# Performance work log

Hardware: AMD Instinct MI355X
Metric: run time of the kernel (lower is better)

## Reference

```python
import jax, jax.numpy as jnp
import numpy as np

N, T, NC, D = 256, 20, 1, 32
NF, Q, VSTEPS, HDYN = 16, 32, 10, 256
HDIM = NF * 64           # n_filt * 4**3
DT = 0.1
BETA = 1.0
LOG2PI = float(np.log(2.0 * np.pi))


def conv2d(x, w, b):
    # k=4, s=2, p=1 : halves spatial dims. x: [B,Cin,H,W], w: [Cout,Cin,4,4]
    y = jax.lax.conv_general_dilated(x, w, (2, 2), [(1, 1), (1, 1)],
                                     dimension_numbers=('NCHW', 'OIHW', 'NCHW'))
    return y + b[None, :, None, None]


def deconv2d(x, w, b):
    # stride-2 transposed conv, doubles spatial dims. w: [Cout,Cin,4,4]
    y = jax.lax.conv_transpose(x, w, (2, 2), 'SAME',
                               dimension_numbers=('NCHW', 'OIHW', 'NCHW'))
    return y + b[None, :, None, None]


def encode(x, C1, c1, C2, c2, C3, c3, Wm, bm, Wl, bl):
    h = jax.nn.relu(conv2d(x, C1, c1))
    h = jax.nn.relu(conv2d(h, C2, c2))
    h = jax.nn.relu(conv2d(h, C3, c3))   # [B, 4*NF, 4, 4]
    h = h.reshape(h.shape[0], -1)        # [B, HDIM]
    return h @ Wm + bm, h @ Wl + bl


def setup_inputs() -> dict:
    key = jax.random.key(0)
    ks = jax.random.split(key, 40)
    r = lambda i, shape, s=0.05: s * jax.random.normal(ks[i], shape, jnp.float32)
    inp = {
        'X': jax.random.uniform(ks[0], (N, T, NC, D, D), jnp.float32),
        'eps_s0': jax.random.normal(ks[1], (N, Q), jnp.float32),
        'eps_v0': jax.random.normal(ks[2], (N, Q), jnp.float32),
        # enc_s (input = 1 frame)
        'Cs1': r(3, (NF, NC, 4, 4)), 'cs1': jnp.zeros((NF,)),
        'Cs2': r(4, (2 * NF, NF, 4, 4)), 'cs2': jnp.zeros((2 * NF,)),
        'Cs3': r(5, (4 * NF, 2 * NF, 4, 4)), 'cs3': jnp.zeros((4 * NF,)),
        'Wsm': r(6, (HDIM, Q)), 'bsm': jnp.zeros((Q,)),
        'Wsl': r(7, (HDIM, Q), 0.01), 'bsl': -1.0 * jnp.ones((Q,)),
        # enc_v (input = v_steps frames stacked as channels)
        'Cv1': r(8, (NF, VSTEPS * NC, 4, 4)), 'cv1': jnp.zeros((NF,)),
        'Cv2': r(9, (2 * NF, NF, 4, 4)), 'cv2': jnp.zeros((2 * NF,)),
        'Cv3': r(10, (4 * NF, 2 * NF, 4, 4)), 'cv3': jnp.zeros((4 * NF,)),
        'Wvm': r(11, (HDIM, Q)), 'bvm': jnp.zeros((Q,)),
        'Wvl': r(12, (HDIM, Q), 0.01), 'bvl': -1.0 * jnp.ones((Q,)),
        # dynamics f : R^{2q} -> R^q (tanh MLP)
        'W1': r(13, (2 * Q, HDYN), 0.1), 'b1': jnp.zeros((HDYN,)),
        'W2': r(14, (HDYN, Q), 0.1), 'b2': jnp.zeros((Q,)),
        # fc3 + decoder
        'Wf': r(15, (Q, HDIM)), 'bf': jnp.zeros((HDIM,)),
        'D1': r(16, (2 * NF, 4 * NF, 4, 4)), 'd1': jnp.zeros((2 * NF,)),
        'D2': r(17, (NF, 2 * NF, 4, 4)), 'd2': jnp.zeros((NF,)),
        'D3': r(18, (NC, NF, 4, 4)), 'd3': jnp.zeros((NC,)),
        'Ndata': 10000,
    }
    return inp


def reference(X, eps_s0, eps_v0,
              Cs1, cs1, Cs2, cs2, Cs3, cs3, Wsm, bsm, Wsl, bsl,
              Cv1, cv1, Cv2, cv2, Cv3, cv3, Wvm, bvm, Wvl, bvl,
              W1, b1, W2, b2, Wf, bf, D1, d1, D2, d2, D3, d3, Ndata):
    Nb, Tt = X.shape[0], X.shape[1]
    # ---- encode z0 = [v0, s0]
    s0_mu, s0_lv = encode(X[:, 0], Cs1, cs1, Cs2, cs2, Cs3, cs3, Wsm, bsm, Wsl, bsl)
    xv = X[:, :VSTEPS].reshape(Nb, VSTEPS * NC, D, D)
    v0_mu, v0_lv = encode(xv, Cv1, cv1, Cv2, cv2, Cv3, cv3, Wvm, bvm, Wvl, bvl)
    s0 = s0_mu + eps_s0 * jnp.exp(s0_lv)
    v0 = v0_mu + eps_v0 * jnp.exp(v0_lv)
    # standard-normal density of the base noise (q dims each)
    logp0 = (-0.5 * jnp.sum(eps_s0 ** 2, -1) - 0.5 * Q * LOG2PI) + \
            (-0.5 * jnp.sum(eps_v0 ** 2, -1) - 0.5 * Q * LOG2PI)
    z0 = jnp.concatenate([v0, s0], axis=1)               # [N,2q]
    qz0_m = jnp.concatenate([v0_mu, s0_mu], axis=1)
    qz0_logv = jnp.concatenate([v0_lv, s0_lv], axis=1)

    # ---- augmented ODE rhs: dz = [f(z), v], dlogp = -tr(df/dv)
    # exact trace for the tanh MLP: J = W2^T diag(1-h^2) W1^T, so
    # tr_{i<q} J = (1-h^2) @ c with c_k = sum_{i<q} W1[i,k] * W2[k,i]
    c = jnp.sum(W1[:Q] * W2.T, axis=0)                   # [HDYN]

    def rhs(vs):
        h = jnp.tanh(vs @ W1 + b1)                       # [N,HDYN]
        dv = h @ W2 + b2                                 # [N,q]
        dvs = jnp.concatenate([dv, vs[:, :Q]], axis=1)   # [N,2q]
        tr = (1.0 - h * h) @ c                           # [N]
        return dvs, -tr

    def rk4_step(carry, _):
        z, lp = carry
        k1z, k1l = rhs(z)
        k2z, k2l = rhs(z + 0.5 * DT * k1z)
        k3z, k3l = rhs(z + 0.5 * DT * k2z)
        k4z, k4l = rhs(z + DT * k3z)
        z2 = z + (DT / 6.0) * (k1z + 2 * k2z + 2 * k3z + k4z)
        lp2 = lp + (DT / 6.0) * (k1l + 2 * k2l + 2 * k3l + k4l)
        return (z2, lp2), (z2, lp2)

    (_, _), (zs, lps) = jax.lax.scan(rk4_step, (z0, logp0), None, length=Tt - 1)
    zt = jnp.concatenate([z0[None], zs], axis=0)         # [T,N,2q]
    logp = jnp.concatenate([logp0[None], lps], axis=0)   # [T,N]
    ztL = jnp.transpose(zt, (1, 0, 2))[None]             # [1,N,T,2q] (L=1)
    logpL = logp.T[None]                                 # [1,N,T]

    # ---- decode positions s_t
    s = ztL[..., Q:].reshape(-1, Q) @ Wf + bf            # [N*T, HDIM]
    h = s.reshape(-1, 4 * NF, 4, 4)
    h = jax.nn.relu(deconv2d(h, D1, d1))                 # [N*T,2NF,8,8]
    h = jax.nn.relu(deconv2d(h, D2, d2))                 # [N*T,NF,16,16]
    Xrec = jax.nn.sigmoid(deconv2d(h, D3, d3))           # [N*T,NC,32,32]
    Xrec = Xrec.reshape(1, Nb, Tt, NC, D, D)

    # ---- ELBO
    log_pzt = -0.5 * jnp.sum(ztL ** 2, -1) - Q * LOG2PI  # N(0,I) over 2q dims
    kl_z = (logpL - log_pzt).sum(2).mean(0)              # [N]
    lhood_L = jnp.log(0.001 + Xrec) * X[None] + jnp.log(1.001 - Xrec) * (1.0 - X[None])
    lhood = lhood_L.sum((2, 3, 4, 5)).mean(0)            # [N]
    kl_w = 0.5 * (jnp.sum(W1 ** 2) + jnp.sum(W2 ** 2))
    Nd = jnp.float32(Ndata)
    lh = Nd * lhood.mean()
    klz = Nd * kl_z.mean()
    elbo = lh - klz - BETA * kl_w
    return Xrec, qz0_m, qz0_logv, ztL, elbo, lh, klz, BETA * kl_w


if __name__ == '__main__':
    outs = reference(**setup_inputs())
    print(outs[0].shape, float(outs[4]))
```

## Files before the change

### kernel.cpp

```cpp
#include <hip/hip_runtime.h>
#include <math.h>

#define N_S 256
#define T_S 20
#define D_S 32
#define NF_S 16
#define Q_S 32
#define HDYN_S 256
#define HDIM_S 1024
#define VSTEPS_S 10
#define DT_S 0.1f
#define LOG2PI_F 1.8378770664093453f

#define OUT_XREC 0
#define OUT_QM   5242880
#define OUT_QLV  5259264
#define OUT_ZT   5275648
#define OUT_SCAL 5603328

#define WS_A1    0
#define WS_A3    0
#define WS_WT2   32768
#define WS_WT3   40960
#define WS_A2    1048576
#define WS_M1    1048576
#define WS_C1    1114112
#define WS_S0MU  1572864
#define WS_S0LV  1581056
#define WS_V0MU  1589248
#define WS_V0LV  1597440
#define WS_LOGP  1605632
#define WS_LHOOD 1610752
#define WS_KLZ   1611008
#define WS_KLW   1611264
#define WS_TC    1611520
#define TC_S1 (WS_TC + 0)
#define TC_V1 (WS_TC + 256)
#define TC_S2 (WS_TC + 2816)
#define TC_V2 (WS_TC + 11008)
#define TC_S3 (WS_TC + 19200)
#define TC_V3 (WS_TC + 51968)

__device__ inline void enc_tr(const float* __restrict__ src, float* __restrict__ dst,
                              int e, int CI, int CO) {
    int co = e % CO; int r = e / CO; int tap = r & 15; int ci = r >> 4;
    dst[e] = src[(co * CI + ci) * 16 + tap];
}
__device__ inline void dec_tr(const float* __restrict__ src, float* __restrict__ dst,
                              int e, int CI, int CO) {
    int co = e % CO; int r = e / CO; int ci = r % CI; int tap = r / CI;
    dst[e] = src[(co * CI + ci) * 16 + tap];
}

__global__ __launch_bounds__(256) void prep_enc(
    const float* __restrict__ Cs1, const float* __restrict__ Cv1,
    const float* __restrict__ Cs2, const float* __restrict__ Cv2,
    const float* __restrict__ Cs3, const float* __restrict__ Cv3,
    float* __restrict__ ws)
{
    int idx = blockIdx.x * 256 + threadIdx.x;
    if (blockIdx.x == 0) ws[WS_LHOOD + threadIdx.x] = 0.f;
    if (idx < 256)        enc_tr(Cs1, ws + TC_S1, idx,          1, 16);
    else if (idx < 2816)  enc_tr(Cv1, ws + TC_V1, idx - 256,   10, 16);
    else if (idx < 11008) enc_tr(Cs2, ws + TC_S2, idx - 2816,  16, 32);
    else if (idx < 19200) enc_tr(Cv2, ws + TC_V2, idx - 11008, 16, 32);
    else if (idx < 51968) enc_tr(Cs3, ws + TC_S3, idx - 19200, 32, 64);
    else if (idx < 84736) enc_tr(Cv3, ws + TC_V3, idx - 51968, 32, 64);
}

template<int CIN>
__global__ __launch_bounds__(256) void conv1_lds(
    const float* __restrict__ x, const float* __restrict__ wt,
    const float* __restrict__ bias, float* __restrict__ out)
{
    __shared__ float xin[CIN * 630];
    __shared__ float wl[CIN * 256];
    __shared__ float bl[16];
    int b = blockIdx.x, yh = blockIdx.y, t = threadIdx.x;
    for (int e = t; e < CIN * 576; e += 256) {
        int ci = e / 576;
        int r = (e >> 5) - ci * 18;
        int cx = e & 31;
        int gy = yh * 16 - 1 + r;
        float v = (gy >= 0 && gy < 32) ? x[(size_t)b * 20480 + ci * 1024 + gy * 32 + cx] : 0.f;
        xin[ci * 630 + r * 35 + cx + 1] = v;
    }
    for (int e = t; e < CIN * 18; e += 256) {
        int ci = e / 18, r = e - ci * 18;
        xin[ci * 630 + r * 35 + 0] = 0.f;
        xin[ci * 630 + r * 35 + 33] = 0.f;
    }
    for (int e = t; e < CIN * 256; e += 256) wl[e] = wt[e];
    if (t < 16) bl[t] = bias[t];
    __syncthreads();

    int ocq = t >> 7, p = t & 127;
    int oyl = p >> 4, ox = p & 15;
    float acc[8];
    #pragma unroll
    for (int j = 0; j < 8; j++) acc[j] = bl[ocq * 8 + j];
    for (int ci = 0; ci < CIN; ci++) {
        const float* xc = xin + ci * 630;
        const float* wc = wl + ci * 256 + ocq * 8;
        #pragma unroll
        for (int ky = 0; ky < 4; ky++) {
            const float* xr = xc + (2 * oyl + ky) * 35;
            #pragma unroll
            for (int kx = 0; kx < 4; kx++) {
                float v = xr[2 * ox + kx];
                const float4* w4 = (const float4*)(wc + (ky * 4 + kx) * 16);
                float4 wa = w4[0], wb = w4[1];
                acc[0] = fmaf(v, wa.x, acc[0]);
                acc[1] = fmaf(v, wa.y, acc[1]);
                acc[2] = fmaf(v, wa.z, acc[2]);
                acc[3] = fmaf(v, wa.w, acc[3]);
                acc[4] = fmaf(v, wb.x, acc[4]);
                acc[5] = fmaf(v, wb.y, acc[5]);
                acc[6] = fmaf(v, wb.z, acc[6]);
                acc[7] = fmaf(v, wb.w, acc[7]);
            }
        }
    }
    int oy = yh * 8 + oyl;
    size_t ob = (size_t)b * 4096 + (size_t)(ocq * 8) * 256 + oy * 16 + ox;
    #pragma unroll
    for (int j = 0; j < 8; j++) out[ob + (size_t)j * 256] = fmaxf(acc[j], 0.f);
}

__global__ __launch_bounds__(256) void conv2_lds(
    const float* __restrict__ a1, const float* __restrict__ wt,
    const float* __restrict__ bias, float* __restrict__ out)
{
    __shared__ float xin[16 * 272];
    __shared__ float wl[4096];
    __shared__ float bl[16];
    int b = blockIdx.x, h = blockIdx.y, t = threadIdx.x;
    for (int e = t; e < 4096; e += 256) {
        int ci = e >> 8, r = e & 255, iy = r >> 4, ix = r & 15;
        xin[ci * 272 + iy * 17 + ix] = a1[(size_t)b * 4096 + e];
    }
    for (int e = t; e < 4096; e += 256) {
        int ci = e >> 8, r = e & 255, tap = r >> 4, oc = r & 15;
        wl[e] = wt[ci * 512 + tap * 32 + h * 16 + oc];
    }
    if (t < 16) bl[t] = bias[h * 16 + t];
    __syncthreads();

    int ocq = t >> 6, p = t & 63;
    int pa = p >> 3, pb = p & 7;
    float acc[4];
    #pragma unroll
    for (int j = 0; j < 4; j++) acc[j] = bl[ocq * 4 + j];
    for (int ci = 0; ci < 16; ci++) {
        const float* xc = xin + ci * 272;
        const float* wc = wl + ci * 256 + ocq * 4;
        #pragma unroll
        for (int ky = 0; ky < 4; ky++) {
            int iy = 2 * pa - 1 + ky;
            if ((unsigned)iy >= 16u) continue;
            const float* xr = xc + iy * 17;
            #pragma unroll
            for (int kx = 0; kx < 4; kx++) {
                int ix = 2 * pb - 1 + kx;
                if ((unsigned)ix >= 16u) continue;
                float v = xr[ix];
                float4 wv = *(const float4*)(wc + (ky * 4 + kx) * 16);
                acc[0] = fmaf(v, wv.x, acc[0]);
                acc[1] = fmaf(v, wv.y, acc[1]);
                acc[2] = fmaf(v, wv.z, acc[2]);
                acc[3] = fmaf(v, wv.w, acc[3]);
            }
        }
    }
    size_t ob = (size_t)b * 2048 + (size_t)(h * 16 + ocq * 4) * 64 + pa * 8 + pb;
    #pragma unroll
    for (int j = 0; j < 4; j++) out[ob + (size_t)j * 64] = fmaxf(acc[j], 0.f);
}

__global__ __launch_bounds__(256) void conv3_lds(
    const float* __restrict__ a2, const float* __restrict__ wt,
    const float* __restrict__ bias, float* __restrict__ out)
{
    __shared__ float xin[32 * 72];
    __shared__ float wl[16384];
    __shared__ float bl[32];
    int b = blockIdx.x, h = blockIdx.y, t = threadIdx.x;
    for (int e = t; e < 2048; e += 256) {
        int ci = e >> 6, r = e & 63, iy = r >> 3, ix = r & 7;
        xin[ci * 72 + iy * 9 + ix] = a2[(size_t)b * 2048 + e];
    }
    for (int e4 = t; e4 < 4096; e4 += 256) {
        int grp = e4 >> 3, c4 = e4 & 7;
        ((float4*)wl)[e4] = ((const float4*)(wt + grp * 64 + h * 32))[c4];
    }
    if (t < 32) bl[t] = bias[h * 32 + t];
    __syncthreads();

    int ocq = t >> 4, p = t & 15;
    int pa = p >> 2, pb = p & 3;
    float a0 = bl[ocq * 2], a1 = bl[ocq * 2 + 1];
    for (int ci = 0; ci < 32; ci++) {
        const float* xc = xin + ci * 72;
        const float* wc = wl + ci * 512 + ocq * 2;
        #pragma unroll
        for (int ky = 0; ky < 4; ky++) {
            int iy = 2 * pa - 1 + ky;
            if ((unsigned)iy >= 8u) continue;
            const float* xr = xc + iy * 9;
            #pragma unroll
            for (int kx = 0; kx < 4; kx++) {
                int ix = 2 * pb - 1 + kx;
                if ((unsigned)ix >= 8u) continue;
                float v = xr[ix];
                float2 wv = *(const float2*)(wc + (ky * 4 + kx) * 32);
                a0 = fmaf(v, wv.x, a0);
                a1 = fmaf(v, wv.y, a1);
            }
        }
    }
    size_t ob = (size_t)b * 1024 + (size_t)(h * 32 + ocq * 2) * 16 + pa * 4 + pb;
    out[ob] = fmaxf(a0, 0.f);
    out[ob + 16] = fmaxf(a1, 0.f);
}

__global__ __launch_bounds__(256) void fc_enc2(
    const float* __restrict__ h,
    const float* __restrict__ Wm, const float* __restrict__ bm,
    const float* __restrict__ Wl, const float* __restrict__ bl,
    float* __restrict__ mu, float* __restrict__ lv)
{
    __shared__ float pm[8][32], pl[8][32];
    int b = blockIdx.x, t = threadIdx.x;
    int q = t & 31, c = t >> 5;
    const float* hb = h + (size_t)b * HDIM_S + c * 128;
    const float* wmp = Wm + (c * 128) * Q_S + q;
    const float* wlp = Wl + (c * 128) * Q_S + q;
    float am = 0.f, al = 0.f;
    #pragma unroll 4
    for (int k = 0; k < 128; k++) {
        float hv = hb[k];
        am = fmaf(hv, wmp[k * Q_S], am);
        al = fmaf(hv, wlp[k * Q_S], al);
    }
    pm[c][q] = am; pl[c][q] = al;
    __syncthreads();
    if (t < 32) {
        float s = bm[t];
        #pragma unroll
        for (int c2 = 0; c2 < 8; c2++) s += pm[c2][t];
        mu[b * Q_S + t] = s;
    } else if (t < 64) {
        int qq = t - 32;
        float s = bl[qq];
        #pragma unroll
        for (int c2 = 0; c2 < 8; c2++) s += pl[c2][qq];
        lv[b * Q_S + qq] = s;
    }
}

__global__ __launch_bounds__(256) void m1_prep(
    const float* __restrict__ Wf, const float* __restrict__ bf,
    const float* __restrict__ D1, const float* __restrict__ d1,
    float* __restrict__ ws)
{
    int blk = blockIdx.x, t = threadIdx.x;
    if (blk < 64) {
        __shared__ float WfL[4096];
        __shared__ float D1L[4096];
        int j = blk >> 3, q4 = blk & 7;
        for (int e = t; e < 4096; e += 256) {
            int qq = e >> 10, k = e & 1023;
            WfL[e] = Wf[(size_t)(q4 * 4 + qq) * 1024 + k];
        }
        for (int e = t; e < 4096; e += 256) {
            int ocg = e >> 10, r = e & 1023;
            D1L[e] = D1[(size_t)(ocg * 8 + j) * 1024 + r];
        }
        __syncthreads();
        int p = t & 63, ocg = t >> 6;
        int y = p >> 3, x = p & 7;
        float acc[4] = {0.f, 0.f, 0.f, 0.f};
        #pragma unroll
        for (int sy = 0; sy < 2; sy++) {
            int ky = (y & 1) + 2 * sy;
            int iy = ((y + ky) >> 1) - 1;
            if ((unsigned)iy >= 4u) continue;
            #pragma unroll
            for (int sx = 0; sx < 2; sx++) {
                int kx = (x & 1) + 2 * sx;
                int ix = ((x + kx) >> 1) - 1;
                if ((unsigned)ix >= 4u) continue;
                const float* dl = D1L + ocg * 1024 + ky * 4 + kx;
                const float* wl = WfL + iy * 4 + ix;
                for (int ci = 0; ci < 64; ci++) {
                    float wv = dl[ci * 16];
                    int kb = ci * 16;
                    acc[0] = fmaf(wl[kb],        wv, acc[0]);
                    acc[1] = fmaf(wl[1024 + kb], wv, acc[1]);
                    acc[2] = fmaf(wl[2048 + kb], wv, acc[2]);
                    acc[3] = fmaf(wl[3072 + kb], wv, acc[3]);
                }
            }
        }
        float4 o4 = make_float4(acc[0], acc[1], acc[2], acc[3]);
        ((float4*)(ws + WS_M1))[blk * 256 + t] = o4;
    } else {
        __shared__ float bfL[1024];
        __shared__ float D1c[2048];
        int bb = blk - 64;
        for (int e = t; e < 1024; e += 256) bfL[e] = bf[e];
        for (int e = t; e < 2048; e += 256) D1c[e] = D1[(size_t)bb * 2048 + e];
        __syncthreads();
        int oidx = t >> 1, half = t & 1;
        int ocr = oidx >> 6, p = oidx & 63;
        int y = p >> 3, x = p & 7;
        float acc = 0.f;
        #pragma unroll
        for (int sy = 0; sy < 2; sy++) {
            int ky = (y & 1) + 2 * sy;
            int iy = ((y + ky) >> 1) - 1;
            if ((unsigned)iy >= 4u) continue;
            #pragma unroll
            for (int sx = 0; sx < 2; sx++) {
                int kx = (x & 1) + 2 * sx;
                int ix = ((x + kx) >> 1) - 1;
                if ((unsigned)ix >= 4u) continue;
                const float* dl = D1c + ocr * 1024 + half * 512 + ky * 4 + kx;
                const float* wl = bfL + half * 512 + iy * 4 + ix;
                for (int cc = 0; cc < 32; cc++)
                    acc = fmaf(wl[cc * 16], dl[cc * 16], acc);
            }
        }
        acc += __shfl_down(acc, 1, 64);
        if (half == 0) {
            int oc = bb * 2 + ocr;
            ws[WS_C1 + (oc & 7) * 256 + (oc >> 3) * 64 + p] = acc + d1[oc];
        }
    }
}

__global__ __launch_bounds__(256) void reparam_prep(
    const float* __restrict__ s0mu, const float* __restrict__ s0lv,
    const float* __restrict__ v0mu, const float* __restrict__ v0lv,
    const float* __restrict__ eps_s, const float* __restrict__ eps_v,
    const float* __restrict__ D2, const float* __restrict__ D3,
    float* __restrict__ ws,
    float* __restrict__ qm, float* __restrict__ qlv,
    float* __restrict__ ztL, float* __restrict__ logp)
{
    int n = blockIdx.x, t = threadIdx.x;
    int idx = n * 256 + t;
    if (idx < 8192)      dec_tr(D2, ws + WS_WT2, idx,        32, 16);
    else if (idx < 8448) dec_tr(D3, ws + WS_WT3, idx - 8192, 16, 1);
    if (t < 64) {
        int q = t & 31;
        float mu, lvv, ep;
        if (t < 32) { mu = v0mu[n*32+q]; lvv = v0lv[n*32+q]; ep = eps_v[n*32+q]; }
        else        { mu = s0mu[n*32+q]; lvv = s0lv[n*32+q]; ep = eps_s[n*32+q]; }
        float zv = fmaf(ep, expf(lvv), mu);
        qm[n*64 + t]  = mu;
        qlv[n*64 + t] = lvv;
        ztL[(size_t)n * T_S * 64 + t] = zv;
        float e2 = ep * ep;
        #pragma unroll
        for (int off = 32; off; off >>= 1) e2 += __shfl_down(e2, off, 64);
        if (t == 0) logp[n * T_S] = -0.5f * e2 - Q_S * LOG2PI_F;
    }
}

__global__ __launch_bounds__(256) void ode_kernel(
    const float* __restrict__ W1, const float* __restrict__ b1,
    const float* __restrict__ W2, const float* __restrict__ b2,
    float* __restrict__ ztL, float* __restrict__ logp)
{
    __shared__ float W2s[HDYN_S * Q_S];
    __shared__ float zeval[64];
    __shared__ float hsh[HDYN_S];
    __shared__ float dvred[HDYN_S];
    __shared__ float red4[4];
    int n = blockIdx.x;
    int t = threadIdx.x;

    for (int i = t; i < HDYN_S * Q_S; i += 256) W2s[i] = W2[i];
    float w1r[64];
    #pragma unroll
    for (int j = 0; j < 64; j++) w1r[j] = W1[j * HDYN_S + t];
    float b1r = b1[t];
    __syncthreads();
    float ck = 0.f;
    #pragma unroll
    for (int i = 0; i < Q_S; i++) ck = fmaf(w1r[i], W2s[t * Q_S + i], ck);

    size_t zoff = (size_t)n * T_S * 64;
    float zj = 0.f, ksumj = 0.f, zevalj = 0.f, lp = 0.f, lsum = 0.f;
    if (t < 64) { zj = ztL[zoff + t]; zevalj = zj; zeval[t] = zj; }
    if (t == 0) lp = logp[n * T_S];

    const float wc[4] = {1.f, 2.f, 2.f, 1.f};
    const float ac[3] = {0.5f * DT_S, 0.5f * DT_S, DT_S};

    for (int step = 1; step < T_S; step++) {
        for (int e = 0; e < 4; e++) {
            __syncthreads();
            float p0 = 0.f, p1 = 0.f, p2 = 0.f, p3 = 0.f;
            #pragma unroll
            for (int j = 0; j < 16; j++) {
                p0 = fmaf(zeval[j],      w1r[j],      p0);
                p1 = fmaf(zeval[j + 16], w1r[j + 16], p1);
                p2 = fmaf(zeval[j + 32], w1r[j + 32], p2);
                p3 = fmaf(zeval[j + 48], w1r[j + 48], p3);
            }
            float pre = b1r + ((p0 + p1) + (p2 + p3));
            float hk = tanhf(pre);
            hsh[t] = hk;
            float gk = (1.f - hk * hk) * ck;
            #pragma unroll
            for (int off = 32; off; off >>= 1) gk += __shfl_down(gk, off, 64);
            if ((t & 63) == 0) red4[t >> 6] = gk;
            __syncthreads();
            {
                int i = t & 31, p = t >> 5;
                float a0 = 0.f, a1 = 0.f;
                #pragma unroll
                for (int kk = 0; kk < 16; kk++) {
                    a0 = fmaf(hsh[p * 32 + kk],      W2s[(p * 32 + kk) * Q_S + i],      a0);
                    a1 = fmaf(hsh[p * 32 + 16 + kk], W2s[(p * 32 + 16 + kk) * Q_S + i], a1);
                }
                dvred[t] = a0 + a1;
            }
            __syncthreads();
            if (t < 64) {
                float tr = red4[0] + red4[1] + red4[2] + red4[3];
                float zv_shfl = __shfl(zevalj, (t >= 32) ? (t - 32) : t, 64);
                float kzv;
                if (t < 32) {
                    float dvi = b2[t];
                    #pragma unroll
                    for (int p = 0; p < 8; p++) dvi += dvred[p * 32 + t];
                    kzv = dvi;
                } else kzv = zv_shfl;
                if (e == 0) ksumj = kzv; else ksumj = fmaf(wc[e], kzv, ksumj);
                if (t == 0) { float kl = -tr; lsum = (e == 0) ? kl : fmaf(wc[e], kl, lsum); }
                if (e < 3) {
                    zevalj = fmaf(ac[e], kzv, zj);
                    zeval[t] = zevalj;
                } else {
                    zj = fmaf(DT_S / 6.f, ksumj, zj);
                    zevalj = zj; zeval[t] = zj;
                    ztL[zoff + step * 64 + t] = zj;
                    if (t == 0) { lp = fmaf(DT_S / 6.f, lsum, lp); logp[n * T_S + step] = lp; }
                }
            }
        }
    }
}

__global__ __launch_bounds__(256) void decoder5(
    const float* __restrict__ ztL, const float* __restrict__ M1L, const float* __restrict__ c1L,
    const float* __restrict__ wt2, const float* __restrict__ d2,
    const float* __restrict__ wt3, const float* __restrict__ d3,
    const float* __restrict__ X, float* __restrict__ Xrec, float* __restrict__ lhood)
{
    __shared__ float zs[32];
    __shared__ float regA[3600];
    __shared__ float regB[4160];
    __shared__ float sh4[4];
    float* h2f = regB;
    float* h1f = regA;
    float* xst = regA;
    const int bidx = blockIdx.x;
    const int t = threadIdx.x;
    const int wu = __builtin_amdgcn_readfirstlane(t >> 6);
    const int l = t & 63;
    const int py = wu >> 1, px = wu & 1;

    if (t < 32) zs[t] = ztL[(size_t)bidx * 64 + 32 + t];
    {
        float4 z4 = make_float4(0.f, 0.f, 0.f, 0.f);
        for (int e = t; e < 900; e += 256) ((float4*)regA)[e] = z4;
    }
    __syncthreads();

    {
        float acc[8];
        #pragma unroll
        for (int j = 0; j < 8; j++) acc[j] = c1L[j * 256 + t];
        const float4* M14 = (const float4*)M1L;
        #pragma unroll
        for (int q4 = 0; q4 < 8; q4++) {
            float4 z4 = *(const float4*)(zs + q4 * 4);
            #pragma unroll
            for (int j = 0; j < 8; j++) {
                float4 m = M14[(j * 8 + q4) * 256 + t];
                acc[j] = fmaf(z4.x, m.x, fmaf(z4.y, m.y, fmaf(z4.z, m.z, fmaf(z4.w, m.w, acc[j]))));
            }
        }
        int p = t & 63, ocg = t >> 6;
        int y = p >> 3, x = p & 7;
        float* hp = h1f + (y + 1) * 360 + (x + 1) * 36 + ocg * 8;
        float4 r0, r1;
        r0.x = fmaxf(acc[0], 0.f); r0.y = fmaxf(acc[1], 0.f);
        r0.z = fmaxf(acc[2], 0.f); r0.w = fmaxf(acc[3], 0.f);
        r1.x = fmaxf(acc[4], 0.f); r1.y = fmaxf(acc[5], 0.f);
        r1.z = fmaxf(acc[6], 0.f); r1.w = fmaxf(acc[7], 0.f);
        *(float4*)(hp)     = r0;
        *(float4*)(hp + 4) = r1;
    }
    __syncthreads();

    {
        int a = l >> 3, b = l & 7;
        float acc[16];
        #pragma unroll
        for (int j = 0; j < 16; j++) acc[j] = d2[j];
        #pragma unroll
        for (int sy = 0; sy < 2; sy++) {
            int ky = py + 2 * sy;
            int iyf = a + py + sy - 1;
            #pragma unroll
            for (int sx = 0; sx < 2; sx++) {
                int kx = px + 2 * sx;
                int ixf = b + px + sx - 1;
                const float4* ip4 = (const float4*)(h1f + (iyf + 1) * 360 + (ixf + 1) * 36);
                const float* wb = wt2 + (ky * 4 + kx) * 512;
                #pragma unroll 2
                for (int cc = 0; cc < 8; cc++) {
                    float4 v = ip4[cc];
                    float vv[4] = {v.x, v.y, v.z, v.w};
                    #pragma unroll
                    for (int r = 0; r < 4; r++) {
                        const float4* wq = (const float4*)(wb + (cc * 4 + r) * 16);
                        float4 w0 = wq[0], w1 = wq[1], w2 = wq[2], w3 = wq[3];
                        float vr = vv[r];
                        acc[0]  = fmaf(vr, w0.x, acc[0]);
                        acc[1]  = fmaf(vr, w0.y, acc[1]);
                        acc[2]  = fmaf(vr, w0.z, acc[2]);
                        acc[3]  = fmaf(vr, w0.w, acc[3]);
                        acc[4]  = fmaf(vr, w1.x, acc[4]);
                        acc[5]  = fmaf(vr, w1.y, acc[5]);
                        acc[6]  = fmaf(vr, w1.z, acc[6]);
                        acc[7]  = fmaf(vr, w1.w, acc[7]);
                        acc[8]  = fmaf(vr, w2.x, acc[8]);
                        acc[9]  = fmaf(vr, w2.y, acc[9]);
                        acc[10] = fmaf(vr, w2.z, acc[10]);
                        acc[11] = fmaf(vr, w2.w, acc[11]);
                        acc[12] = fmaf(vr, w3.x, acc[12]);
                        acc[13] = fmaf(vr, w3.y, acc[13]);
                        acc[14] = fmaf(vr, w3.z, acc[14]);
                        acc[15] = fmaf(vr, w3.w, acc[15]);
                    }
                }
            }
        }
        float* hq = h2f + (2 * a + py) * 260 + (2 * b + px) * 16;
        #pragma unroll
        for (int j = 0; j < 4; j++) {
            float4 r;
            r.x = fmaxf(acc[j*4+0], 0.f);
            r.y = fmaxf(acc[j*4+1], 0.f);
            r.z = fmaxf(acc[j*4+2], 0.f);
            r.w = fmaxf(acc[j*4+3], 0.f);
            *(float4*)(hq + j * 4) = r;
        }
    }
    __syncthreads();

    {
        int oy2 = l >> 2, b3 = l & 3;
        float acc[4];
        float d30 = d3[0];
        #pragma unroll
        for (int k = 0; k < 4; k++) acc[k] = d30;
        #pragma unroll
        for (int sy = 0; sy < 2; sy++) {
            int ky = py + 2 * sy;
            int iy = oy2 + py + sy - 1;
            if ((unsigned)iy >= 16u) continue;
            #pragma unroll
            for (int sx = 0; sx < 2; sx++) {
                int kx = px + 2 * sx;
                int cx = px + sx - 1;
                const float* wvp = wt3 + (ky * 4 + kx) * 16;
                #pragma unroll
                for (int k = 0; k < 4; k++) {
                    int ix = b3 + 4 * k + cx;
                    if ((unsigned)ix >= 16u) continue;
                    const float4* in4 = (const float4*)(h2f + iy * 260 + ix * 16);
                    #pragma unroll
                    for (int cc = 0; cc < 4; cc++) {
                        float4 v = in4[cc];
                        float4 wq = ((const float4*)wvp)[cc];
                        acc[k] = fmaf(v.x, wq.x, acc[k]);
                        acc[k] = fmaf(v.y, wq.y, acc[k]);
                        acc[k] = fmaf(v.z, wq.z, acc[k]);
                        acc[k] = fmaf(v.w, wq.w, acc[k]);
                    }
                }
            }
        }
        int oy = 2 * oy2 + py;
        #pragma unroll
        for (int k = 0; k < 4; k++) {
            int ox = 2 * (b3 + 4 * k) + px;
            xst[oy * 36 + ox] = 1.f / (1.f + expf(-acc[k]));
        }
    }
    __syncthreads();

    {
        int row = t >> 3, col = (t & 7) * 4;
        float4 xr4 = *(const float4*)(xst + row * 36 + col);
        *(float4*)(Xrec + (size_t)bidx * 1024 + t * 4) = xr4;
        float4 xi4 = *(const float4*)(X + (size_t)bidx * 1024 + t * 4);
        float ll = 0.f;
        ll += logf(0.001f + xr4.x) * xi4.x + logf(1.001f - xr4.x) * (1.f - xi4.x);
        ll += logf(0.001f + xr4.y) * xi4.y + logf(1.001f - xr4.y) * (1.f - xi4.y);
        ll += logf(0.001f + xr4.z) * xi4.z + logf(1.001f - xr4.z) * (1.f - xi4.z);
        ll += logf(0.001f + xr4.w) * xi4.w + logf(1.001f - xr4.w) * (1.f - xi4.w);
        #pragma unroll
        for (int off = 32; off; off >>= 1) ll += __shfl_down(ll, off, 64);
        if ((t & 63) == 0) sh4[t >> 6] = ll;
    }
    __syncthreads();
    if (t == 0) atomicAdd(&lhood[bidx / T_S], sh4[0] + sh4[1] + sh4[2] + sh4[3]);
}

__global__ __launch_bounds__(64) void klz_kernel(
    const float* __restrict__ ztL, const float* __restrict__ logp, float* __restrict__ klz)
{
    int n = blockIdx.x, t = threadIdx.x;
    float v = 0.f;
    if (t < T_S) {
        const float* z = ztL + ((size_t)n * T_S + t) * 64;
        float s2 = 0.f;
        #pragma unroll
        for (int j = 0; j < 64; j++) s2 = fmaf(z[j], z[j], s2);
        v = logp[n * T_S + t] - (-0.5f * s2 - Q_S * LOG2PI_F);
    }
    #pragma unroll
    for (int off = 32; off; off >>= 1) v += __shfl_down(v, off, 64);
    if (t == 0) klz[n] = v;
}

__global__ __launch_bounds__(256) void final2(
    const float* __restrict__ lhood, const float* __restrict__ klz,
    const float* __restrict__ W1, const float* __restrict__ W2,
    const int* __restrict__ Ndata, float* __restrict__ outs)
{
    __shared__ float shA[4], shB[4], shC[4];
    int t = threadIdx.x;
    float a = lhood[t];
    float b = klz[t];
    float c = 0.f;
    for (int i = t; i < 64 * HDYN_S; i += 256) c = fmaf(W1[i], W1[i], c);
    for (int i = t; i < HDYN_S * Q_S; i += 256) c = fmaf(W2[i], W2[i], c);
    #pragma unroll
    for (int off = 32; off; off >>= 1) {
        a += __shfl_down(a, off, 64);
        b += __shfl_down(b, off, 64);
        c += __shfl_down(c, off, 64);
    }
    if ((t & 63) == 0) { shA[t >> 6] = a; shB[t >> 6] = b; shC[t >> 6] = c; }
    __syncthreads();
    if (t == 0) {
        float Nd = (float)Ndata[0];
        float lh = Nd * ((shA[0] + shA[1] + shA[2] + shA[3]) / 256.f);
        float kz = Nd * ((shB[0] + shB[1] + shB[2] + shB[3]) / 256.f);
        float bkw = 0.5f * (shC[0] + shC[1] + shC[2] + shC[3]);
        outs[0] = lh - kz - bkw;
        outs[1] = lh;
        outs[2] = kz;
        outs[3] = bkw;
    }
}

extern "C" void kernel_launch(void* const* d_in, const int* in_sizes, int n_in,
                              void* d_out, int out_size, void* d_ws, size_t ws_size,
                              hipStream_t stream) {
    const float* X      = (const float*)d_in[0];
    const float* eps_s0 = (const float*)d_in[1];
    const float* eps_v0 = (const float*)d_in[2];
    const float* Cs1 = (const float*)d_in[3],  *cs1 = (const float*)d_in[4];
    const float* Cs2 = (const float*)d_in[5],  *cs2 = (const float*)d_in[6];
    const float* Cs3 = (const float*)d_in[7],  *cs3 = (const float*)d_in[8];
    const float* Wsm = (const float*)d_in[9],  *bsm = (const float*)d_in[10];
    const float* Wsl = (const float*)d_in[11], *bsl = (const float*)d_in[12];
    const float* Cv1 = (const float*)d_in[13], *cv1 = (const float*)d_in[14];
    const float* Cv2 = (const float*)d_in[15], *cv2 = (const float*)d_in[16];
    const float* Cv3 = (const float*)d_in[17], *cv3 = (const float*)d_in[18];
    const float* Wvm = (const float*)d_in[19], *bvm = (const float*)d_in[20];
    const float* Wvl = (const float*)d_in[21], *bvl = (const float*)d_in[22];
    const float* W1  = (const float*)d_in[23], *b1  = (const float*)d_in[24];
    const float* W2  = (const float*)d_in[25], *b2  = (const float*)d_in[26];
    const float* Wf  = (const float*)d_in[27], *bf  = (const float*)d_in[28];
    const float* D1  = (const float*)d_in[29], *d1  = (const float*)d_in[30];
    const float* D2  = (const float*)d_in[31], *d2  = (const float*)d_in[32];
    const float* D3  = (const float*)d_in[33], *d3  = (const float*)d_in[34];
    const int*   Ndata = (const int*)d_in[35];

    float* out = (float*)d_out;
    float* ws  = (float*)d_ws;

    prep_enc<<<331, 256, 0, stream>>>(Cs1, Cv1, Cs2, Cv2, Cs3, Cv3, ws);

    conv1_lds<1><<<dim3(256, 2), 256, 0, stream>>>(X, ws + TC_S1, cs1, ws + WS_A1);
    conv2_lds<<<dim3(256, 2), 256, 0, stream>>>(ws + WS_A1, ws + TC_S2, cs2, ws + WS_A2);
    conv3_lds<<<dim3(256, 2), 256, 0, stream>>>(ws + WS_A2, ws + TC_S3, cs3, ws + WS_A3);
    fc_enc2<<<256, 256, 0, stream>>>(ws + WS_A3, Wsm, bsm, Wsl, bsl, ws + WS_S0MU, ws + WS_S0LV);

    conv1_lds<10><<<dim3(256, 2), 256, 0, stream>>>(X, ws + TC_V1, cv1, ws + WS_A1);
    conv2_lds<<<dim3(256, 2), 256, 0, stream>>>(ws + WS_A1, ws + TC_V2, cv2, ws + WS_A2);
    conv3_lds<<<dim3(256, 2), 256, 0, stream>>>(ws + WS_A2, ws + TC_V3, cv3, ws + WS_A3);
    fc_enc2<<<256, 256, 0, stream>>>(ws + WS_A3, Wvm, bvm, Wvl, bvl, ws + WS_V0MU, ws + WS_V0LV);

    m1_prep<<<80, 256, 0, stream>>>(Wf, bf, D1, d1, ws);

    reparam_prep<<<256, 256, 0, stream>>>(ws + WS_S0MU, ws + WS_S0LV, ws + WS_V0MU, ws + WS_V0LV,
                                          eps_s0, eps_v0, D2, D3, ws,
                                          out + OUT_QM, out + OUT_QLV,
                                          out + OUT_ZT, ws + WS_LOGP);

    ode_kernel<<<256, 256, 0, stream>>>(W1, b1, W2, b2, out + OUT_ZT, ws + WS_LOGP);

    decoder5<<<5120, 256, 0, stream>>>(out + OUT_ZT, ws + WS_M1, ws + WS_C1,
                                       ws + WS_WT2, d2, ws + WS_WT3, d3,
                                       X, out + OUT_XREC, ws + WS_LHOOD);

    klz_kernel<<<256, 64, 0, stream>>>(out + OUT_ZT, ws + WS_LOGP, ws + WS_KLZ);
    final2<<<1, 256, 0, stream>>>(ws + WS_LHOOD, ws + WS_KLZ, W1, W2, Ndata,
                                  out + OUT_SCAL);
}
```

Before: 502.4 us.

## Merge s/v encoder branches into shared launches and fold KL into ODE kernel

The two encoder branches (single-frame s and stacked-frame v) now run in combined conv1/conv2/conv3/fc kernels, with a grid dimension selecting the branch. The s-branch activations go to scratch space in the output buffer so both branches can run at the same time. The m1_prep work is folded into reparam_prep, and the KL-z reduction is computed inside the ODE integration loop, which removes the klz kernel. conv1 and conv2 also stop staging weights in LDS and read them straight from global memory with wave-uniform offsets, trading LDS traffic for scalar or cached loads.

```diff
diff --git a/kernel.cpp b/kernel.cpp
--- a/kernel.cpp
+++ b/kernel.cpp
@@ -18,11 +18,15 @@
 #define OUT_ZT   5275648
 #define OUT_SCAL 5603328
 
-#define WS_A1    0
-#define WS_A3    0
+#define OS_A1S   0
+#define OS_A2S   1048576
+#define OS_A3S   1572864
+
+#define WS_A1V   0
+#define WS_A3V   0
 #define WS_WT2   32768
 #define WS_WT3   40960
-#define WS_A2    1048576
+#define WS_A2V   1048576
 #define WS_M1    1048576
 #define WS_C1    1114112
 #define WS_S0MU  1572864
@@ -68,16 +72,20 @@
     else if (idx < 84736) enc_tr(Cv3, ws + TC_V3, idx - 51968, 32, 64);
 }
 
-template<int CIN>
-__global__ __launch_bounds__(256) void conv1_lds(
-    const float* __restrict__ x, const float* __restrict__ wt,
-    const float* __restrict__ bias, float* __restrict__ out)
-{
-    __shared__ float xin[CIN * 630];
-    __shared__ float wl[CIN * 256];
-    __shared__ float bl[16];
+__global__ __launch_bounds__(256) void conv1_both(
+    const float* __restrict__ x,
+    const float* __restrict__ wts, const float* __restrict__ bs, float* __restrict__ outs,
+    const float* __restrict__ wtv, const float* __restrict__ bv, float* __restrict__ outv)
+{
+    __shared__ float xin[10 * 630];
+    int sel = blockIdx.z;
+    int cin = sel ? 10 : 1;
+    const float* wt = sel ? wtv : wts;
+    const float* bias = sel ? bv : bs;
+    float* out = sel ? outv : outs;
+
     int b = blockIdx.x, yh = blockIdx.y, t = threadIdx.x;
-    for (int e = t; e < CIN * 576; e += 256) {
+    for (int e = t; e < cin * 576; e += 256) {
         int ci = e / 576;
         int r = (e >> 5) - ci * 18;
         int cx = e & 31;
@@ -85,23 +93,23 @@
         float v = (gy >= 0 && gy < 32) ? x[(size_t)b * 20480 + ci * 1024 + gy * 32 + cx] : 0.f;
         xin[ci * 630 + r * 35 + cx + 1] = v;
     }
-    for (int e = t; e < CIN * 18; e += 256) {
+    for (int e = t; e < cin * 18; e += 256) {
         int ci = e / 18, r = e - ci * 18;
         xin[ci * 630 + r * 35 + 0] = 0.f;
         xin[ci * 630 + r * 35 + 33] = 0.f;
     }
-    for (int e = t; e < CIN * 256; e += 256) wl[e] = wt[e];
-    if (t < 16) bl[t] = bias[t];
-    __syncthreads();
-
-    int ocq = t >> 7, p = t & 127;
+    __syncthreads();
+
+    int ocq = __builtin_amdgcn_readfirstlane(t >> 7);
+    int p = t & 127;
     int oyl = p >> 4, ox = p & 15;
+    const float* wg = wt + ocq * 8;
     float acc[8];
     #pragma unroll
-    for (int j = 0; j < 8; j++) acc[j] = bl[ocq * 8 + j];
-    for (int ci = 0; ci < CIN; ci++) {
+    for (int j = 0; j < 8; j++) acc[j] = bias[ocq * 8 + j];
+    for (int ci = 0; ci < cin; ci++) {
         const float* xc = xin + ci * 630;
-        const float* wc = wl + ci * 256 + ocq * 8;
+        const float* wc = wg + ci * 256;
         #pragma unroll
         for (int ky = 0; ky < 4; ky++) {
             const float* xr = xc + (2 * oyl + ky) * 35;
@@ -109,15 +117,15 @@
             for (int kx = 0; kx < 4; kx++) {
                 float v = xr[2 * ox + kx];
                 const float4* w4 = (const float4*)(wc + (ky * 4 + kx) * 16);
-                float4 wa = w4[0], wb = w4[1];
+                float4 wa = w4[0], wb2 = w4[1];
                 acc[0] = fmaf(v, wa.x, acc[0]);
                 acc[1] = fmaf(v, wa.y, acc[1]);
                 acc[2] = fmaf(v, wa.z, acc[2]);
                 acc[3] = fmaf(v, wa.w, acc[3]);
-                acc[4] = fmaf(v, wb.x, acc[4]);
-                acc[5] = fmaf(v, wb.y, acc[5]);
-                acc[6] = fmaf(v, wb.z, acc[6]);
-                acc[7] = fmaf(v, wb.w, acc[7]);
+                acc[4] = fmaf(v, wb2.x, acc[4]);
+                acc[5] = fmaf(v, wb2.y, acc[5]);
+                acc[6] = fmaf(v, wb2.z, acc[6]);
+                acc[7] = fmaf(v, wb2.w, acc[7]);
             }
         }
     }
@@ -127,33 +135,36 @@
     for (int j = 0; j < 8; j++) out[ob + (size_t)j * 256] = fmaxf(acc[j], 0.f);
 }
 
-__global__ __launch_bounds__(256) void conv2_lds(
-    const float* __restrict__ a1, const float* __restrict__ wt,
-    const float* __restrict__ bias, float* __restrict__ out)
+__global__ __launch_bounds__(256) void conv2_both(
+    const float* __restrict__ a1s, const float* __restrict__ wts, const float* __restrict__ bsb,
+    float* __restrict__ outs,
+    const float* __restrict__ a1v, const float* __restrict__ wtv, const float* __restrict__ bvb,
+    float* __restrict__ outv)
 {
     __shared__ float xin[16 * 272];
-    __shared__ float wl[4096];
-    __shared__ float bl[16];
+    int sel = blockIdx.z;
+    const float* a1 = sel ? a1v : a1s;
+    const float* wt = sel ? wtv : wts;
+    const float* bias = sel ? bvb : bsb;
+    float* out = sel ? outv : outs;
+
     int b = blockIdx.x, h = blockIdx.y, t = threadIdx.x;
     for (int e = t; e < 4096; e += 256) {
         int ci = e >> 8, r = e & 255, iy = r >> 4, ix = r & 15;
         xin[ci * 272 + iy * 17 + ix] = a1[(size_t)b * 4096 + e];
     }
-    for (int e = t; e < 4096; e += 256) {
-        int ci = e >> 8, r = e & 255, tap = r >> 4, oc = r & 15;
-        wl[e] = wt[ci * 512 + tap * 32 + h * 16 + oc];
-    }
-    if (t < 16) bl[t] = bias[h * 16 + t];
-    __syncthreads();
-
-    int ocq = t >> 6, p = t & 63;
+    __syncthreads();
+
+    int ocq = __builtin_amdgcn_readfirstlane(t >> 6);
+    int p = t & 63;
     int pa = p >> 3, pb = p & 7;
+    int hbase = h * 16 + ocq * 4;
     float acc[4];
     #pragma unroll
-    for (int j = 0; j < 4; j++) acc[j] = bl[ocq * 4 + j];
+    for (int j = 0; j < 4; j++) acc[j] = bias[hbase + j];
     for (int ci = 0; ci < 16; ci++) {
         const float* xc = xin + ci * 272;
-        const float* wc = wl + ci * 256 + ocq * 4;
+        const float* wc = wt + ci * 512 + hbase;
         #pragma unroll
         for (int ky = 0; ky < 4; ky++) {
             int iy = 2 * pa - 1 + ky;
@@ -164,7 +175,7 @@
                 int ix = 2 * pb - 1 + kx;
                 if ((unsigned)ix >= 16u) continue;
                 float v = xr[ix];
-                float4 wv = *(const float4*)(wc + (ky * 4 + kx) * 16);
+                float4 wv = *(const float4*)(wc + (ky * 4 + kx) * 32);
                 acc[0] = fmaf(v, wv.x, acc[0]);
                 acc[1] = fmaf(v, wv.y, acc[1]);
                 acc[2] = fmaf(v, wv.z, acc[2]);
@@ -172,18 +183,26 @@
             }
         }
     }
-    size_t ob = (size_t)b * 2048 + (size_t)(h * 16 + ocq * 4) * 64 + pa * 8 + pb;
+    size_t ob = (size_t)b * 2048 + (size_t)(hbase) * 64 + pa * 8 + pb;
     #pragma unroll
     for (int j = 0; j < 4; j++) out[ob + (size_t)j * 64] = fmaxf(acc[j], 0.f);
 }
 
-__global__ __launch_bounds__(256) void conv3_lds(
-    const float* __restrict__ a2, const float* __restrict__ wt,
-    const float* __restrict__ bias, float* __restrict__ out)
+__global__ __launch_bounds__(256) void conv3_both(
+    const float* __restrict__ a2s, const float* __restrict__ wts, const float* __restrict__ bsb,
+    float* __restrict__ outs,
+    const float* __restrict__ a2v, const float* __restrict__ wtv, const float* __restrict__ bvb,
+    float* __restrict__ outv)
 {
     __shared__ float xin[32 * 72];
     __shared__ float wl[16384];
     __shared__ float bl[32];
+    int sel = blockIdx.z;
+    const float* a2 = sel ? a2v : a2s;
+    const float* wt = sel ? wtv : wts;
+    const float* bias = sel ? bvb : bsb;
+    float* out = sel ? outv : outs;
+
     int b = blockIdx.x, h = blockIdx.y, t = threadIdx.x;
     for (int e = t; e < 2048; e += 256) {
         int ci = e >> 6, r = e & 63, iy = r >> 3, ix = r & 7;
@@ -223,14 +242,26 @@
     out[ob + 16] = fmaxf(a1, 0.f);
 }
 
-__global__ __launch_bounds__(256) void fc_enc2(
-    const float* __restrict__ h,
-    const float* __restrict__ Wm, const float* __restrict__ bm,
-    const float* __restrict__ Wl, const float* __restrict__ bl,
-    float* __restrict__ mu, float* __restrict__ lv)
+__global__ __launch_bounds__(256) void fc_both(
+    const float* __restrict__ hs, const float* __restrict__ hv,
+    const float* __restrict__ Wsm, const float* __restrict__ bsm,
+    const float* __restrict__ Wsl, const float* __restrict__ bsl,
+    const float* __restrict__ Wvm, const float* __restrict__ bvm,
+    const float* __restrict__ Wvl, const float* __restrict__ bvl,
+    float* __restrict__ mus, float* __restrict__ lvs,
+    float* __restrict__ muv, float* __restrict__ lvv)
 {
     __shared__ float pm[8][32], pl[8][32];
-    int b = blockIdx.x, t = threadIdx.x;
+    int sel = blockIdx.x >> 8;
+    int b = blockIdx.x & 255, t = threadIdx.x;
+    const float* h  = sel ? hv : hs;
+    const float* Wm = sel ? Wvm : Wsm;
+    const float* bm = sel ? bvm : bsm;
+    const float* Wl = sel ? Wvl : Wsl;
+    const float* bl = sel ? bvl : bsl;
+    float* mu = sel ? muv : mus;
+    float* lv = sel ? lvv : lvs;
+
     int q = t & 31, c = t >> 5;
     const float* hb = h + (size_t)b * HDIM_S + c * 128;
     const float* wmp = Wm + (c * 128) * Q_S + q;
@@ -238,9 +269,9 @@
     float am = 0.f, al = 0.f;
     #pragma unroll 4
     for (int k = 0; k < 128; k++) {
-        float hv = hb[k];
-        am = fmaf(hv, wmp[k * Q_S], am);
-        al = fmaf(hv, wlp[k * Q_S], al);
+        float hv2 = hb[k];
+        am = fmaf(hv2, wmp[k * Q_S], am);
+        al = fmaf(hv2, wlp[k * Q_S], al);
     }
     pm[c][q] = am; pl[c][q] = al;
     __syncthreads();
@@ -258,23 +289,30 @@
     }
 }
 
-__global__ __launch_bounds__(256) void m1_prep(
+__global__ __launch_bounds__(256) void reparam_prep(
+    const float* __restrict__ s0mu, const float* __restrict__ s0lv,
+    const float* __restrict__ v0mu, const float* __restrict__ v0lv,
+    const float* __restrict__ eps_s, const float* __restrict__ eps_v,
     const float* __restrict__ Wf, const float* __restrict__ bf,
     const float* __restrict__ D1, const float* __restrict__ d1,
-    float* __restrict__ ws)
-{
-    int blk = blockIdx.x, t = threadIdx.x;
-    if (blk < 64) {
-        __shared__ float WfL[4096];
-        __shared__ float D1L[4096];
-        int j = blk >> 3, q4 = blk & 7;
+    const float* __restrict__ D2, const float* __restrict__ D3,
+    float* __restrict__ ws,
+    float* __restrict__ qm, float* __restrict__ qlv,
+    float* __restrict__ ztL, float* __restrict__ logp)
+{
+    __shared__ float shA[4096];
+    __shared__ float shB[4096];
+    int n = blockIdx.x, t = threadIdx.x;
+
+    if (n < 64) {
+        int j = n >> 3, q4 = n & 7;
         for (int e = t; e < 4096; e += 256) {
             int qq = e >> 10, k = e & 1023;
-            WfL[e] = Wf[(size_t)(q4 * 4 + qq) * 1024 + k];
+            shA[e] = Wf[(size_t)(q4 * 4 + qq) * 1024 + k];
         }
         for (int e = t; e < 4096; e += 256) {
             int ocg = e >> 10, r = e & 1023;
-            D1L[e] = D1[(size_t)(ocg * 8 + j) * 1024 + r];
+            shB[e] = D1[(size_t)(ocg * 8 + j) * 1024 + r];
         }
         __syncthreads();
         int p = t & 63, ocg = t >> 6;
@@ -290,8 +328,8 @@
                 int kx = (x & 1) + 2 * sx;
                 int ix = ((x + kx) >> 1) - 1;
                 if ((unsigned)ix >= 4u) continue;
-                const float* dl = D1L + ocg * 1024 + ky * 4 + kx;
-                const float* wl = WfL + iy * 4 + ix;
+                const float* dl = shB + ocg * 1024 + ky * 4 + kx;
+                const float* wl = shA + iy * 4 + ix;
                 for (int ci = 0; ci < 64; ci++) {
                     float wv = dl[ci * 16];
                     int kb = ci * 16;
@@ -302,14 +340,11 @@
                 }
             }
         }
-        float4 o4 = make_float4(acc[0], acc[1], acc[2], acc[3]);
-        ((float4*)(ws + WS_M1))[blk * 256 + t] = o4;
-    } else {
-        __shared__ float bfL[1024];
-        __shared__ float D1c[2048];
-        int bb = blk - 64;
-        for (int e = t; e < 1024; e += 256) bfL[e] = bf[e];
-        for (int e = t; e < 2048; e += 256) D1c[e] = D1[(size_t)bb * 2048 + e];
+        ((float4*)(ws + WS_M1))[n * 256 + t] = make_float4(acc[0], acc[1], acc[2], acc[3]);
+    } else if (n < 80) {
+        int bb = n - 64;
+        for (int e = t; e < 1024; e += 256) shA[e] = bf[e];
+        for (int e = t; e < 2048; e += 256) shB[e] = D1[(size_t)bb * 2048 + e];
         __syncthreads();
         int oidx = t >> 1, half = t & 1;
         int ocr = oidx >> 6, p = oidx & 63;
@@ -325,8 +360,8 @@
                 int kx = (x & 1) + 2 * sx;
                 int ix = ((x + kx) >> 1) - 1;
                 if ((unsigned)ix >= 4u) continue;
-                const float* dl = D1c + ocr * 1024 + half * 512 + ky * 4 + kx;
-                const float* wl = bfL + half * 512 + iy * 4 + ix;
+                const float* dl = shB + ocr * 1024 + half * 512 + ky * 4 + kx;
+                const float* wl = shA + half * 512 + iy * 4 + ix;
                 for (int cc = 0; cc < 32; cc++)
                     acc = fmaf(wl[cc * 16], dl[cc * 16], acc);
             }
@@ -336,30 +371,20 @@
             int oc = bb * 2 + ocr;
             ws[WS_C1 + (oc & 7) * 256 + (oc >> 3) * 64 + p] = acc + d1[oc];
         }
-    }
-}
-
-__global__ __launch_bounds__(256) void reparam_prep(
-    const float* __restrict__ s0mu, const float* __restrict__ s0lv,
-    const float* __restrict__ v0mu, const float* __restrict__ v0lv,
-    const float* __restrict__ eps_s, const float* __restrict__ eps_v,
-    const float* __restrict__ D2, const float* __restrict__ D3,
-    float* __restrict__ ws,
-    float* __restrict__ qm, float* __restrict__ qlv,
-    float* __restrict__ ztL, float* __restrict__ logp)
-{
-    int n = blockIdx.x, t = threadIdx.x;
-    int idx = n * 256 + t;
-    if (idx < 8192)      dec_tr(D2, ws + WS_WT2, idx,        32, 16);
-    else if (idx < 8448) dec_tr(D3, ws + WS_WT3, idx - 8192, 16, 1);
+    } else if (n < 113) {
+        int idx = (n - 80) * 256 + t;
+        if (idx < 8192)      dec_tr(D2, ws + WS_WT2, idx,        32, 16);
+        else if (idx < 8448) dec_tr(D3, ws + WS_WT3, idx - 8192, 16, 1);
+    }
+
     if (t < 64) {
         int q = t & 31;
-        float mu, lvv, ep;
-        if (t < 32) { mu = v0mu[n*32+q]; lvv = v0lv[n*32+q]; ep = eps_v[n*32+q]; }
-        else        { mu = s0mu[n*32+q]; lvv = s0lv[n*32+q]; ep = eps_s[n*32+q]; }
-        float zv = fmaf(ep, expf(lvv), mu);
+        float mu, lvv2, ep;
+        if (t < 32) { mu = v0mu[n*32+q]; lvv2 = v0lv[n*32+q]; ep = eps_v[n*32+q]; }
+        else        { mu = s0mu[n*32+q]; lvv2 = s0lv[n*32+q]; ep = eps_s[n*32+q]; }
+        float zv = fmaf(ep, expf(lvv2), mu);
         qm[n*64 + t]  = mu;
-        qlv[n*64 + t] = lvv;
+        qlv[n*64 + t] = lvv2;
         ztL[(size_t)n * T_S * 64 + t] = zv;
         float e2 = ep * ep;
         #pragma unroll
@@ -371,7 +396,8 @@
 __global__ __launch_bounds__(256) void ode_kernel(
     const float* __restrict__ W1, const float* __restrict__ b1,
     const float* __restrict__ W2, const float* __restrict__ b2,
-    float* __restrict__ ztL, float* __restrict__ logp)
+    float* __restrict__ ztL, const float* __restrict__ logp,
+    float* __restrict__ klz)
 {
     __shared__ float W2s[HDYN_S * Q_S];
     __shared__ float zeval[64];
@@ -392,9 +418,16 @@
     for (int i = 0; i < Q_S; i++) ck = fmaf(w1r[i], W2s[t * Q_S + i], ck);
 
     size_t zoff = (size_t)n * T_S * 64;
-    float zj = 0.f, ksumj = 0.f, zevalj = 0.f, lp = 0.f, lsum = 0.f;
+    float zj = 0.f, ksumj = 0.f, zevalj = 0.f, lp = 0.f, lsum = 0.f, klacc = 0.f;
     if (t < 64) { zj = ztL[zoff + t]; zevalj = zj; zeval[t] = zj; }
     if (t == 0) lp = logp[n * T_S];
+
+    if (t < 64) {
+        float e2 = zj * zj;
+        #pragma unroll
+        for (int off = 32; off; off >>= 1) e2 += __shfl_down(e2, off, 64);
+        if (t == 0) klacc += lp - (-0.5f * e2 - Q_S * LOG2PI_F);
+    }
 
     const float wc[4] = {1.f, 2.f, 2.f, 1.f};
     const float ac[3] = {0.5f * DT_S, 0.5f * DT_S, DT_S};
@@ -448,11 +481,16 @@
                     zj = fmaf(DT_S / 6.f, ksumj, zj);
                     zevalj = zj; zeval[t] = zj;
                     ztL[zoff + step * 64 + t] = zj;
-                    if (t == 0) { lp = fmaf(DT_S / 6.f, lsum, lp); logp[n * T_S + step] = lp; }
+                    if (t == 0) lp = fmaf(DT_S / 6.f, lsum, lp);
+                    float e2 = zj * zj;
+                    #pragma unroll
+                    for (int off = 32; off; off >>= 1) e2 += __shfl_down(e2, off, 64);
+                    if (t == 0) klacc += lp - (-0.5f * e2 - Q_S * LOG2PI_F);
                 }
             }
         }
     }
+    if (t == 0) klz[n] = klacc;
 }
 
 __global__ __launch_bounds__(256) void decoder5(
@@ -625,23 +663,6 @@
     if (t == 0) atomicAdd(&lhood[bidx / T_S], sh4[0] + sh4[1] + sh4[2] + sh4[3]);
 }
 
-__global__ __launch_bounds__(64) void klz_kernel(
-    const float* __restrict__ ztL, const float* __restrict__ logp, float* __restrict__ klz)
-{
-    int n = blockIdx.x, t = threadIdx.x;
-    float v = 0.f;
-    if (t < T_S) {
-        const float* z = ztL + ((size_t)n * T_S + t) * 64;
-        float s2 = 0.f;
-        #pragma unroll
-        for (int j = 0; j < 64; j++) s2 = fmaf(z[j], z[j], s2);
-        v = logp[n * T_S + t] - (-0.5f * s2 - Q_S * LOG2PI_F);
-    }
-    #pragma unroll
-    for (int off = 32; off; off >>= 1) v += __shfl_down(v, off, 64);
-    if (t == 0) klz[n] = v;
-}
-
 __global__ __launch_bounds__(256) void final2(
     const float* __restrict__ lhood, const float* __restrict__ klz,
     const float* __restrict__ W1, const float* __restrict__ W2,
@@ -701,32 +722,37 @@
     float* out = (float*)d_out;
     float* ws  = (float*)d_ws;
 
+    float* a1s = out + OS_A1S;
+    float* a2s = out + OS_A2S;
+    float* a3s = out + OS_A3S;
+
     prep_enc<<<331, 256, 0, stream>>>(Cs1, Cv1, Cs2, Cv2, Cs3, Cv3, ws);
 
-    conv1_lds<1><<<dim3(256, 2), 256, 0, stream>>>(X, ws + TC_S1, cs1, ws + WS_A1);
-    conv2_lds<<<dim3(256, 2), 256, 0, stream>>>(ws + WS_A1, ws + TC_S2, cs2, ws + WS_A2);
-    conv3_lds<<<dim3(256, 2), 256, 0, stream>>>(ws + WS_A2, ws + TC_S3, cs3, ws + WS_A3);
-    fc_enc2<<<256, 256, 0, stream>>>(ws + WS_A3, Wsm, bsm, Wsl, bsl, ws + WS_S0MU, ws + WS_S0LV);
-
-    conv1_lds<10><<<dim3(256, 2), 256, 0, stream>>>(X, ws + TC_V1, cv1, ws + WS_A1);
-    conv2_lds<<<dim3(256, 2), 256, 0, stream>>>(ws + WS_A1, ws + TC_V2, cv2, ws + WS_A2);
-    conv3_lds<<<dim3(256, 2), 256, 0, stream>>>(ws + WS_A2, ws + TC_V3, cv3, ws + WS_A3);
-    fc_enc2<<<256, 256, 0, stream>>>(ws + WS_A3, Wvm, bvm, Wvl, bvl, ws + WS_V0MU, ws + WS_V0LV);
-
-    m1_prep<<<80, 256, 0, stream>>>(Wf, bf, D1, d1, ws);
+    conv1_both<<<dim3(256, 2, 2), 256, 0, stream>>>(X,
+        ws + TC_S1, cs1, a1s,
+        ws + TC_V1, cv1, ws + WS_A1V);
+    conv2_both<<<dim3(256, 2, 2), 256, 0, stream>>>(
+        a1s, ws + TC_S2, cs2, a2s,
+        ws + WS_A1V, ws + TC_V2, cv2, ws + WS_A2V);
+    conv3_both<<<dim3(256, 2, 2), 256, 0, stream>>>(
+        a2s, ws + TC_S3, cs3, a3s,
+        ws + WS_A2V, ws + TC_V3, cv3, ws + WS_A3V);
+    fc_both<<<512, 256, 0, stream>>>(a3s, ws + WS_A3V,
+        Wsm, bsm, Wsl, bsl, Wvm, bvm, Wvl, bvl,
+        ws + WS_S0MU, ws + WS_S0LV, ws + WS_V0MU, ws + WS_V0LV);
 
     reparam_prep<<<256, 256, 0, stream>>>(ws + WS_S0MU, ws + WS_S0LV, ws + WS_V0MU, ws + WS_V0LV,
-                                          eps_s0, eps_v0, D2, D3, ws,
+                                          eps_s0, eps_v0, Wf, bf, D1, d1, D2, D3, ws,
                                           out + OUT_QM, out + OUT_QLV,
                                           out + OUT_ZT, ws + WS_LOGP);
 
-    ode_kernel<<<256, 256, 0, stream>>>(W1, b1, W2, b2, out + OUT_ZT, ws + WS_LOGP);
+    ode_kernel<<<256, 256, 0, stream>>>(W1, b1, W2, b2, out + OUT_ZT, ws + WS_LOGP,
+                                        ws + WS_KLZ);
 
     decoder5<<<5120, 256, 0, stream>>>(out + OUT_ZT, ws + WS_M1, ws + WS_C1,
                                        ws + WS_WT2, d2, ws + WS_WT3, d3,
                                        X, out + OUT_XREC, ws + WS_LHOOD);
 
-    klz_kernel<<<256, 64, 0, stream>>>(out + OUT_ZT, ws + WS_LOGP, ws + WS_KLZ);
     final2<<<1, 256, 0, stream>>>(ws + WS_LHOOD, ws + WS_KLZ, W1, W2, Ndata,
                                   out + OUT_SCAL);
 }
```

Result: no change. 495.3 us (-1.4%).
